# Performance work log

Measured on AMD Instinct MI355X. Metric: run time of the kernel, lower is better.

Reference implementation:

```python
import jax, jax.numpy as jnp
import numpy as np

B, S, H, NH, NKV, D = 1, 2048, 4096, 32, 8, 128
ROPE_BASE = 1000000.0


def setup_inputs() -> dict:
    key = jax.random.key(0)
    k0, k1, k2, k3, k4 = jax.random.split(key, 5)
    hidden_states = jax.random.normal(k0, (B, S, H), dtype=jnp.float32)
    Wq = jax.random.normal(k1, (NH * D, H), dtype=jnp.float32) * 0.02
    Wk = jax.random.normal(k2, (NKV * D, H), dtype=jnp.float32) * 0.02
    Wv = jax.random.normal(k3, (NKV * D, H), dtype=jnp.float32) * 0.02
    Wo = jax.random.normal(k4, (NH * D, NH * D), dtype=jnp.float32) * 0.02
    # RoPE tables (Mistral rope_theta = 1e6), concatenated-halves layout
    inv_freq = 1.0 / (ROPE_BASE ** (jnp.arange(0, D, 2, dtype=jnp.float32) / D))
    pos = jnp.arange(S, dtype=jnp.float32)
    freqs = pos[:, None] * inv_freq[None, :]            # [S, D/2]
    emb = jnp.concatenate([freqs, freqs], axis=-1)       # [S, D]
    cos = jnp.cos(emb)[None]                             # [1, S, D]
    sin = jnp.sin(emb)[None]
    # additive causal mask [1,1,S,S]
    causal = jnp.tril(jnp.ones((S, S), dtype=bool))
    attention_mask = jnp.where(causal, 0.0, -1e9).astype(jnp.float32)[None, None]
    return {"hidden_states": hidden_states, "cos": cos, "sin": sin,
            "attention_mask": attention_mask, "Wq": Wq, "Wk": Wk, "Wv": Wv, "Wo": Wo}


def _rotate_half(x):
    d = x.shape[-1] // 2
    return jnp.concatenate([-x[..., d:], x[..., :d]], axis=-1)


def reference(hidden_states, cos, sin, attention_mask, Wq, Wk, Wv, Wo):
    b, s, _ = hidden_states.shape
    nh = Wq.shape[0] // D
    nkv = Wk.shape[0] // D
    g = nh // nkv  # GQA groups
    scaling = D ** -0.5

    q = (hidden_states @ Wq.T).reshape(b, s, nh, D).transpose(0, 2, 1, 3)   # [b,nh,s,d]
    k = (hidden_states @ Wk.T).reshape(b, s, nkv, D).transpose(0, 2, 1, 3)  # [b,nkv,s,d]
    v = (hidden_states @ Wv.T).reshape(b, s, nkv, D).transpose(0, 2, 1, 3)

    c = cos[:, None]  # [b,1,s,d] broadcast over heads (unsqueeze_dim=1)
    sn = sin[:, None]
    q = q * c + _rotate_half(q) * sn
    k = k * c + _rotate_half(k) * sn

    # grouped-query attention without materializing repeated K/V
    qg = q.reshape(b, nkv, g, s, D)
    attn = jnp.einsum('bkgqd,bksd->bkgqs', qg, k) * scaling
    attn = attn + attention_mask[:, :, None]  # broadcast [1,1,1,s,s]
    w = jax.nn.softmax(attn.astype(jnp.float32), axis=-1).astype(q.dtype)
    out = jnp.einsum('bkgqs,bksd->bkgqd', w, v)  # [b,nkv,g,s,d]
    out = out.reshape(b, nh, s, D).transpose(0, 2, 1, 3).reshape(b, s, nh * D)
    return out @ Wo.T
```

## Files before the change

kernel.cpp:

```cpp
#include <hip/hip_runtime.h>
#include <hip/hip_bf16.h>
#include <cstdint>
#include <cstddef>

#define S_LEN 2048
#define HID   4096
#define NHEAD 32
#define NKVH  8
#define HD    128
#define QKV_STR 6144

typedef __bf16 bf16x8 __attribute__((ext_vector_type(8)));
typedef float  f32x4  __attribute__((ext_vector_type(4)));
typedef float  f32x16 __attribute__((ext_vector_type(16)));
typedef unsigned uint32x2_t __attribute__((ext_vector_type(2)));

__device__ __forceinline__ unsigned short f2bf(float f) {
  union { float f; unsigned int u; } c; c.f = f;
  unsigned int u = c.u;
  return (unsigned short)((u + 0x7fffu + ((u >> 16) & 1u)) >> 16);
}
__device__ __forceinline__ float bf2f(unsigned short b) {
  union { unsigned int u; float f; } c; c.u = ((unsigned int)b) << 16;
  return c.f;
}
__device__ __forceinline__ void gload16(const void* g, void* l) {
  __builtin_amdgcn_global_load_lds((const __attribute__((address_space(1))) void*)g,
                                   (__attribute__((address_space(3))) void*)l, 16, 0, 0);
}

__global__ void cvt_multi(const float* __restrict__ s0, const float* __restrict__ s1,
                          const float* __restrict__ s2, const float* __restrict__ s3,
                          unsigned short* __restrict__ d0, unsigned short* __restrict__ d1,
                          unsigned short* __restrict__ d2, unsigned short* __restrict__ d3,
                          int n0, int n1, int n2, int n3) {
  const float* src; unsigned short* dst; int n;
  switch (blockIdx.y) {
    case 0: src = s0; dst = d0; n = n0; break;
    case 1: src = s1; dst = d1; n = n1; break;
    case 2: src = s2; dst = d2; n = n2; break;
    default: src = s3; dst = d3; n = n3; break;
  }
  int i = blockIdx.x * blockDim.x + threadIdx.x;
  int stride = gridDim.x * blockDim.x;
  for (; i < n; i += stride) {
    float4 v = ((const float4*)src)[i];
    ushort4 o;
    o.x = f2bf(v.x); o.y = f2bf(v.y); o.z = f2bf(v.z); o.w = f2bf(v.w);
    ((ushort4*)dst)[i] = o;
  }
}

template <bool F32OUT>
__global__ __launch_bounds__(256)
void gemm_bt(const unsigned short* __restrict__ A,
             const unsigned short* __restrict__ Bm,
             void* __restrict__ Cout, int N, int K) {
  __shared__ __align__(16) unsigned short lA[3][128 * 32];
  __shared__ __align__(16) unsigned short lB[3][128 * 32];
  const int tid = threadIdx.x;
  const int lane = tid & 63, wid = tid >> 6;
  const int l15 = lane & 15, lg = lane >> 4;
  const int wr = (wid >> 1) * 64, wc = (wid & 1) * 64;
  const int nwg = gridDim.x * 16;
  int bid = blockIdx.x + blockIdx.y * gridDim.x;
  bid = (bid & 7) * (nwg >> 3) + (bid >> 3);
  const int bm = bid & 15, bn = bid >> 4;

  f32x4 acc[4][4] = {};
  const unsigned short* Ab = A + (size_t)bm * 128 * K;
  const unsigned short* Bb = Bm + (size_t)bn * 128 * K;

  auto stage = [&](int t, int buf) {
    const int k0 = t * 32;
#pragma unroll
    for (int i = 0; i < 2; ++i) {
      int c = tid + i * 256;
      int row = c >> 2, sl = c & 3;
      int g = sl ^ ((row >> 1) & 3);
      gload16(Ab + (size_t)row * K + k0 + g * 8, (char*)lA[buf] + c * 16);
      gload16(Bb + (size_t)row * K + k0 + g * 8, (char*)lB[buf] + c * 16);
    }
  };

  const int nt = K / 32;
  stage(0, 0);
  if (nt > 1) stage(1, 1);
  const int swz = (l15 >> 1) & 3;

  int cur = 0;
  for (int t = 0; t < nt; ++t) {
    if (t + 1 < nt) asm volatile("s_waitcnt vmcnt(4)" ::: "memory");
    else            asm volatile("s_waitcnt vmcnt(0)" ::: "memory");
    __builtin_amdgcn_s_barrier();
    __builtin_amdgcn_sched_barrier(0);
    if (t + 2 < nt) { int nb = cur + 2; if (nb >= 3) nb -= 3; stage(t + 2, nb); }
    bf16x8 af[4], bfr[4];
#pragma unroll
    for (int m = 0; m < 4; ++m)
      af[m] = *(const bf16x8*)&lA[cur][(wr + m * 16 + l15) * 32 + ((lg ^ swz) * 8)];
#pragma unroll
    for (int n = 0; n < 4; ++n)
      bfr[n] = *(const bf16x8*)&lB[cur][(wc + n * 16 + l15) * 32 + ((lg ^ swz) * 8)];
#pragma unroll
    for (int m = 0; m < 4; ++m)
#pragma unroll
      for (int n = 0; n < 4; ++n)
        acc[m][n] = __builtin_amdgcn_mfma_f32_16x16x32_bf16(af[m], bfr[n], acc[m][n], 0, 0, 0);
    ++cur; if (cur >= 3) cur -= 3;
  }
  const int r0 = bm * 128 + wr + 4 * lg;
  const int c0 = bn * 128 + wc + l15;
#pragma unroll
  for (int m = 0; m < 4; ++m)
#pragma unroll
    for (int n = 0; n < 4; ++n)
#pragma unroll
      for (int j = 0; j < 4; ++j) {
        size_t idx = (size_t)(r0 + m * 16 + j) * N + (c0 + n * 16);
        if (F32OUT) ((float*)Cout)[idx] = acc[m][n][j];
        else        ((unsigned short*)Cout)[idx] = f2bf(acc[m][n][j]);
      }
}

__global__ __launch_bounds__(256)
void rope_transpose(unsigned short* __restrict__ qkv,
                    const float* __restrict__ cp,
                    const float* __restrict__ sp,
                    unsigned short* __restrict__ VT) {
  __shared__ __align__(16) unsigned short tile[128 * 128];
  const int tid = threadIdx.x;
  const int s0 = blockIdx.x * 128;
  const int kvh = blockIdx.y;
  unsigned short* K = qkv + 4096 + kvh * 128;
#pragma unroll 4
  for (int i = 0; i < 32; ++i) {
    int idx = tid + i * 256;
    int sl = idx >> 6, d = idx & 63;
    float c = cp[(size_t)(s0 + sl) * 128 + d];
    float sn = sp[(size_t)(s0 + sl) * 128 + d];
    size_t base = (size_t)(s0 + sl) * QKV_STR + d;
    float x1 = bf2f(K[base]), x2 = bf2f(K[base + 64]);
    K[base]      = f2bf(x1 * c - x2 * sn);
    K[base + 64] = f2bf(x2 * c + x1 * sn);
  }
  const unsigned short* src = qkv + 5120 + kvh * 128;
#pragma unroll
  for (int i = 0; i < 8; ++i) {
    int c = tid + i * 256;
    int s = c >> 4, dc = c & 15;
    int f = (s ^ (s >> 3)) & 7;
    uint4 v = *(const uint4*)(src + (size_t)(s0 + s) * QKV_STR + dc * 8);
    *(uint4*)&tile[s * 128 + ((dc ^ f) * 8)] = v;
  }
  __syncthreads();
#pragma unroll
  for (int i = 0; i < 8; ++i) {
    int c = tid + i * 256;
    int d = c >> 4, sc = c & 15;
    unsigned short tmp[8];
#pragma unroll
    for (int j = 0; j < 8; ++j) {
      int s = sc * 8 + j;
      int f = (s ^ (s >> 3)) & 7;
      tmp[j] = tile[s * 128 + (((d >> 3) ^ f) * 8) + (d & 7)];
    }
    *(uint4*)(VT + ((size_t)kvh * 128 + d) * S_LEN + s0 + sc * 8) = *(uint4*)tmp;
  }
}

#define CROW(r) (((r) & 3) + 8 * ((r) >> 2) + 4 * hi)
__global__ __launch_bounds__(256, 2)
void flash_attn(const unsigned short* __restrict__ qkv,
                const unsigned short* __restrict__ VT,
                const float* __restrict__ cp,
                const float* __restrict__ sp,
                unsigned short* __restrict__ Og,
                const float* __restrict__ Wo,
                unsigned short* __restrict__ woB) {
  __shared__ __align__(16) unsigned short lK[2 * 64 * 128];
  __shared__ __align__(16) unsigned short lVt[2 * 128 * 64];
  const int tid = threadIdx.x;
  const int lane = tid & 63, w = tid >> 6;
  const int l31 = lane & 31, hi = lane >> 5;
  const int h = blockIdx.y, kvh = h >> 2;
  const int qt = (h & 16) ? blockIdx.x : (15 - blockIdx.x);
  const int nt = 2 * qt + 2;
  const int qminw = qt * 128 + w * 32;
  const int qlane = qminw + l31;
  const int qmaxw = qminw + 31;
  const float S2 = 0.12752960f;

  bf16x8 qf[8];
  {
    const unsigned short* qp = qkv + (size_t)qlane * QKV_STR + h * HD + hi * 8;
#pragma unroll
    for (int ks = 0; ks < 8; ++ks) qf[ks] = *(const bf16x8*)(qp + ks * 16);
    const float* crow = cp + (size_t)qlane * 128 + hi * 8;
    const float* srow = sp + (size_t)qlane * 128 + hi * 8;
#pragma unroll
    for (int ks = 0; ks < 4; ++ks) {
      float4 c0 = *(const float4*)(crow + ks * 16);
      float4 c1 = *(const float4*)(crow + ks * 16 + 4);
      float4 s0 = *(const float4*)(srow + ks * 16);
      float4 s1 = *(const float4*)(srow + ks * 16 + 4);
      float cc[8] = {c0.x, c0.y, c0.z, c0.w, c1.x, c1.y, c1.z, c1.w};
      float ss[8] = {s0.x, s0.y, s0.z, s0.w, s1.x, s1.y, s1.z, s1.w};
#pragma unroll
      for (int j = 0; j < 8; ++j) {
        float x1 = (float)qf[ks][j], x2 = (float)qf[ks + 4][j];
        qf[ks][j]     = (__bf16)(x1 * cc[j] - x2 * ss[j]);
        qf[ks + 4][j] = (__bf16)(x2 * cc[j] + x1 * ss[j]);
      }
    }
  }
  f32x16 accO[4] = {};
  float m_run = -3e38f, l_run = 0.f;

  const unsigned short* Kb0 = qkv + 4096 + kvh * HD;
  const unsigned short* VTh = VT + (size_t)kvh * 128 * S_LEN;

  auto stageK = [&](int t, int buf) {
    const unsigned short* Kb = Kb0 + (size_t)(t * 64) * QKV_STR;
    char* dst = (char*)(lK + buf * (64 * 128));
#pragma unroll
    for (int i = 0; i < 4; ++i) {
      int c = tid + i * 256;
      int row = c >> 4, s = c & 15;
      gload16(Kb + (size_t)row * QKV_STR + ((s ^ (row & 7)) * 8), dst + c * 16);
    }
  };
  auto stageV = [&](int t, int buf) {
    const unsigned short* Vb = VTh + t * 64;
    char* dst = (char*)(lVt + buf * (128 * 64));
#pragma unroll
    for (int i = 0; i < 4; ++i) {
      int c = tid + i * 256;
      int d = c >> 3, s = c & 7;
      gload16(Vb + (size_t)d * S_LEN + ((s ^ (d & 7)) * 8), dst + c * 16);
    }
  };

  stageK(0, 0);
  stageV(0, 0);
  __syncthreads();

  int cur = 0;
  for (int t = 0; t < nt; ++t) {
    const bool pf = (t + 1 < nt);
    if (pf) { stageK(t + 1, cur ^ 1); stageV(t + 1, cur ^ 1); }

#pragma unroll
    for (int c2 = 0; c2 < 2; ++c2) {
      const int kvb = t * 64 + c2 * 32;
      if (kvb > qmaxw) continue;
      f32x16 st = {};
      const unsigned short* lKc = lK + cur * (64 * 128) + c2 * 32 * 128;
      __builtin_amdgcn_s_setprio(1);
#pragma unroll
      for (int ks = 0; ks < 8; ++ks) {
        bf16x8 kf = *(const bf16x8*)&lKc[l31 * 128 + (((ks * 2 + hi) ^ (l31 & 7)) * 8)];
        st = __builtin_amdgcn_mfma_f32_32x32x16_bf16(kf, qf[ks], st, 0, 0, 0);
      }
      __builtin_amdgcn_s_setprio(0);
      if (kvb + 31 > qminw) {
#pragma unroll
        for (int r = 0; r < 16; ++r)
          if (kvb + CROW(r) > qlane) st[r] = -3e38f;
      }
      float t0 = fmaxf(st[0], st[1]),  t1 = fmaxf(st[2], st[3]);
      float t2 = fmaxf(st[4], st[5]),  t3 = fmaxf(st[6], st[7]);
      float t4 = fmaxf(st[8], st[9]),  t5 = fmaxf(st[10], st[11]);
      float t6 = fmaxf(st[12], st[13]), t7 = fmaxf(st[14], st[15]);
      float tm = fmaxf(fmaxf(fmaxf(t0, t1), fmaxf(t2, t3)),
                       fmaxf(fmaxf(t4, t5), fmaxf(t6, t7)));
      tm = fmaxf(tm, __shfl_xor(tm, 32));
      const bool skip = __all((tm - m_run) * S2 <= 8.0f);
      float corr = 1.f;
      if (!skip) {
        float mnew = fmaxf(m_run, tm);
        corr = __builtin_amdgcn_exp2f((m_run - mnew) * S2);
        m_run = mnew;
      }
      const float mS2 = m_run * S2;
      float p[16];
#pragma unroll
      for (int r = 0; r < 16; ++r) p[r] = __builtin_amdgcn_exp2f(st[r] * S2 - mS2);
      float s0b = (p[0] + p[1]) + (p[2] + p[3]);
      float s1b = (p[4] + p[5]) + (p[6] + p[7]);
      float s2b = (p[8] + p[9]) + (p[10] + p[11]);
      float s3b = (p[12] + p[13]) + (p[14] + p[15]);
      float rsum = (s0b + s1b) + (s2b + s3b);
      rsum += __shfl_xor(rsum, 32);
      l_run = l_run * corr + rsum;
      if (!skip) {
#pragma unroll
        for (int db = 0; db < 4; ++db) accO[db] = accO[db] * corr;
      }
      unsigned wpk[8];
#pragma unroll
      for (int i = 0; i < 8; ++i) {
        __hip_bfloat162 b2 = __float22bfloat162_rn(float2{p[2 * i], p[2 * i + 1]});
        wpk[i] = *(unsigned*)&b2;
      }
      int4 pa0i, pa1i;
#if __has_builtin(__builtin_amdgcn_permlane32_swap)
      uint32x2_t r0 = __builtin_amdgcn_permlane32_swap(wpk[0], wpk[2], false, false);
      uint32x2_t r1 = __builtin_amdgcn_permlane32_swap(wpk[1], wpk[3], false, false);
      uint32x2_t r2 = __builtin_amdgcn_permlane32_swap(wpk[4], wpk[6], false, false);
      uint32x2_t r3 = __builtin_amdgcn_permlane32_swap(wpk[5], wpk[7], false, false);
      pa0i.x = (int)r0.x; pa0i.y = (int)r1.x; pa0i.z = (int)r0.y; pa0i.w = (int)r1.y;
      pa1i.x = (int)r2.x; pa1i.y = (int)r3.x; pa1i.z = (int)r2.y; pa1i.w = (int)r3.y;
#else
      unsigned xpk[8];
#pragma unroll
      for (int i = 0; i < 8; ++i) xpk[i] = (unsigned)__shfl_xor((int)wpk[i], 32);
      pa0i.x = hi ? (int)xpk[2] : (int)wpk[0]; pa0i.y = hi ? (int)xpk[3] : (int)wpk[1];
      pa0i.z = hi ? (int)wpk[2] : (int)xpk[0]; pa0i.w = hi ? (int)wpk[3] : (int)xpk[1];
      pa1i.x = hi ? (int)xpk[6] : (int)wpk[4]; pa1i.y = hi ? (int)xpk[7] : (int)wpk[5];
      pa1i.z = hi ? (int)wpk[6] : (int)xpk[4]; pa1i.w = hi ? (int)wpk[7] : (int)xpk[5];
#endif
      bf16x8 pa0 = *(bf16x8*)&pa0i, pa1 = *(bf16x8*)&pa1i;
      const unsigned short* lVc = lVt + cur * (128 * 64);
      __builtin_amdgcn_s_setprio(1);
#pragma unroll
      for (int db = 0; db < 4; ++db) {
        int d = db * 32 + l31;
#pragma unroll
        for (int ks2 = 0; ks2 < 2; ++ks2) {
          int ck = c2 * 4 + ks2 * 2 + hi;
          bf16x8 vf = *(const bf16x8*)&lVc[d * 64 + ((ck ^ (d & 7)) * 8)];
          accO[db] = __builtin_amdgcn_mfma_f32_32x32x16_bf16(vf, ks2 ? pa1 : pa0, accO[db], 0, 0, 0);
        }
      }
      __builtin_amdgcn_s_setprio(0);
    }
    __syncthreads();
    cur ^= 1;
  }

  const float invl = 1.0f / l_run;
  unsigned short* orow = Og + (size_t)(qt * 128 + w * 32 + l31) * HID + h * HD;
#pragma unroll
  for (int db = 0; db < 4; ++db)
#pragma unroll
    for (int rr = 0; rr < 4; ++rr) {
      int d0 = db * 32 + rr * 8 + 4 * hi;
      ushort4 o;
      o.x = f2bf(accO[db][rr * 4 + 0] * invl);
      o.y = f2bf(accO[db][rr * 4 + 1] * invl);
      o.z = f2bf(accO[db][rr * 4 + 2] * invl);
      o.w = f2bf(accO[db][rr * 4 + 3] * invl);
      *(ushort4*)(orow + d0) = o;
    }

  {
    const int gb = blockIdx.y * gridDim.x + blockIdx.x;
    const int total = HID * HID / 4;
    for (int i = gb * 256 + tid; i < total; i += 512 * 256) {
      float4 v = ((const float4*)Wo)[i];
      ushort4 o;
      o.x = f2bf(v.x); o.y = f2bf(v.y); o.z = f2bf(v.z); o.w = f2bf(v.w);
      ((ushort4*)woB)[i] = o;
    }
  }
}

extern "C" void kernel_launch(void* const* d_in, const int* in_sizes, int n_in,
                              void* d_out, int out_size, void* d_ws, size_t ws_size,
                              hipStream_t stream) {
  const float* hs   = (const float*)d_in[0];
  const float* cosp = (const float*)d_in[1];
  const float* sinp = (const float*)d_in[2];
  const float* Wq = (const float*)d_in[4];
  const float* Wk = (const float*)d_in[5];
  const float* Wv = (const float*)d_in[6];
  const float* Wo = (const float*)d_in[7];
  float* out = (float*)d_out;

  uint8_t* ws = (uint8_t*)d_ws;
  size_t off = 0;
  auto alloc = [&](size_t bytes) { void* p = ws + off; off += bytes; return p; };
  unsigned short* hidB  = (unsigned short*)alloc((size_t)S_LEN * HID * 2);
  unsigned short* wqkvB = (unsigned short*)alloc((size_t)QKV_STR * HID * 2);
  unsigned short* woB   = (unsigned short*)alloc((size_t)HID * HID * 2);
  unsigned short* qkvB  = (unsigned short*)alloc((size_t)S_LEN * QKV_STR * 2);
  unsigned short* aoB   = (unsigned short*)alloc((size_t)S_LEN * HID * 2);
  unsigned short* vtB   = (unsigned short*)alloc((size_t)NKVH * HD * S_LEN * 2);

  cvt_multi<<<dim3(1024, 4), 256, 0, stream>>>(
      hs, Wq, Wk, Wv,
      hidB, wqkvB, wqkvB + (size_t)HID * HID, wqkvB + (size_t)(HID + 1024) * HID,
      S_LEN * HID / 4, HID * HID / 4, 1024 * HID / 4, 1024 * HID / 4);

  gemm_bt<false><<<dim3(QKV_STR / 128, S_LEN / 128), 256, 0, stream>>>(
      hidB, wqkvB, qkvB, QKV_STR, HID);

  rope_transpose<<<dim3(S_LEN / 128, NKVH), 256, 0, stream>>>(qkvB, cosp, sinp, vtB);

  flash_attn<<<dim3(S_LEN / 128, NHEAD), 256, 0, stream>>>(
      qkvB, vtB, cosp, sinp, aoB, Wo, woB);

  gemm_bt<true><<<dim3(HID / 128, S_LEN / 128), 256, 0, stream>>>(
      aoB, woB, out, HID, HID);
}
```

Baseline: 335.7 us.

## Fuse K RoPE and V transpose into QKV GEMM epilogue

Removes the separate rope_transpose kernel. In the QKV GEMM epilogue, tiles covering K columns stage the accumulators through shared memory and apply RoPE before storing, and tiles covering V columns write straight into the transposed VT layout. This saves one launch and a full read/write pass over K and V. In exchange the epilogue for those blocks gains extra shared-memory traffic and scattered cos/sin loads, and the V stores are 8-byte strided writes.

```diff
diff --git a/kernel.cpp b/kernel.cpp
--- a/kernel.cpp
+++ b/kernel.cpp
@@ -51,13 +51,16 @@
   }
 }
 
-template <bool F32OUT>
+template <bool F32OUT, bool EPIFUSE>
 __global__ __launch_bounds__(256)
 void gemm_bt(const unsigned short* __restrict__ A,
              const unsigned short* __restrict__ Bm,
-             void* __restrict__ Cout, int N, int K) {
-  __shared__ __align__(16) unsigned short lA[3][128 * 32];
-  __shared__ __align__(16) unsigned short lB[3][128 * 32];
+             void* __restrict__ Cout, int N, int K,
+             const float* __restrict__ cp, const float* __restrict__ sp,
+             unsigned short* __restrict__ VT) {
+  __shared__ __align__(16) unsigned short lsmem[2 * 3 * 128 * 32];
+  unsigned short (*lA)[128 * 32] = (unsigned short (*)[128 * 32])lsmem;
+  unsigned short (*lB)[128 * 32] = (unsigned short (*)[128 * 32])(lsmem + 3 * 128 * 32);
   const int tid = threadIdx.x;
   const int lane = tid & 63, wid = tid >> 6;
   const int l15 = lane & 15, lg = lane >> 4;
@@ -111,6 +114,55 @@
   }
   const int r0 = bm * 128 + wr + 4 * lg;
   const int c0 = bn * 128 + wc + l15;
+
+  if (EPIFUSE && bn >= 40) {
+    const int kvh = bn - 40;
+#pragma unroll
+    for (int n = 0; n < 4; ++n) {
+      int d = wc + n * 16 + l15;
+      unsigned short* vrow = VT + ((size_t)kvh * 128 + d) * S_LEN + bm * 128 + wr + 4 * lg;
+#pragma unroll
+      for (int m = 0; m < 4; ++m) {
+        ushort4 o;
+        o.x = f2bf(acc[m][n][0]); o.y = f2bf(acc[m][n][1]);
+        o.z = f2bf(acc[m][n][2]); o.w = f2bf(acc[m][n][3]);
+        *(ushort4*)(vrow + m * 16) = o;
+      }
+    }
+    return;
+  }
+  if (EPIFUSE && bn >= 32) {
+    __syncthreads();
+    unsigned short* scr = lsmem;
+    const int sl0 = wr + 4 * lg;
+#pragma unroll
+    for (int m = 0; m < 4; ++m)
+#pragma unroll
+      for (int n = 0; n < 4; ++n) {
+        int d = wc + n * 16 + l15;
+#pragma unroll
+        for (int j = 0; j < 4; ++j)
+          scr[(sl0 + m * 16 + j) * 128 + d] = f2bf(acc[m][n][j]);
+      }
+    __syncthreads();
+#pragma unroll
+    for (int m = 0; m < 4; ++m)
+#pragma unroll
+      for (int n = 0; n < 4; ++n) {
+        int d = wc + n * 16 + l15;
+#pragma unroll
+        for (int j = 0; j < 4; ++j) {
+          int sl = sl0 + m * 16 + j;
+          float x = bf2f(scr[sl * 128 + d]);
+          float pr = bf2f(scr[sl * 128 + (d ^ 64)]);
+          size_t crow = (size_t)(bm * 128 + sl) * 128 + (d & 63);
+          float c = cp[crow], sn = sp[crow];
+          float o = (d < 64) ? (x * c - pr * sn) : (x * c + pr * sn);
+          ((unsigned short*)Cout)[(size_t)(bm * 128 + sl) * N + bn * 128 + d] = f2bf(o);
+        }
+      }
+    return;
+  }
 #pragma unroll
   for (int m = 0; m < 4; ++m)
 #pragma unroll
@@ -121,52 +173,6 @@
         if (F32OUT) ((float*)Cout)[idx] = acc[m][n][j];
         else        ((unsigned short*)Cout)[idx] = f2bf(acc[m][n][j]);
       }
-}
-
-__global__ __launch_bounds__(256)
-void rope_transpose(unsigned short* __restrict__ qkv,
-                    const float* __restrict__ cp,
-                    const float* __restrict__ sp,
-                    unsigned short* __restrict__ VT) {
-  __shared__ __align__(16) unsigned short tile[128 * 128];
-  const int tid = threadIdx.x;
-  const int s0 = blockIdx.x * 128;
-  const int kvh = blockIdx.y;
-  unsigned short* K = qkv + 4096 + kvh * 128;
-#pragma unroll 4
-  for (int i = 0; i < 32; ++i) {
-    int idx = tid + i * 256;
-    int sl = idx >> 6, d = idx & 63;
-    float c = cp[(size_t)(s0 + sl) * 128 + d];
-    float sn = sp[(size_t)(s0 + sl) * 128 + d];
-    size_t base = (size_t)(s0 + sl) * QKV_STR + d;
-    float x1 = bf2f(K[base]), x2 = bf2f(K[base + 64]);
-    K[base]      = f2bf(x1 * c - x2 * sn);
-    K[base + 64] = f2bf(x2 * c + x1 * sn);
-  }
-  const unsigned short* src = qkv + 5120 + kvh * 128;
-#pragma unroll
-  for (int i = 0; i < 8; ++i) {
-    int c = tid + i * 256;
-    int s = c >> 4, dc = c & 15;
-    int f = (s ^ (s >> 3)) & 7;
-    uint4 v = *(const uint4*)(src + (size_t)(s0 + s) * QKV_STR + dc * 8);
-    *(uint4*)&tile[s * 128 + ((dc ^ f) * 8)] = v;
-  }
-  __syncthreads();
-#pragma unroll
-  for (int i = 0; i < 8; ++i) {
-    int c = tid + i * 256;
-    int d = c >> 4, sc = c & 15;
-    unsigned short tmp[8];
-#pragma unroll
-    for (int j = 0; j < 8; ++j) {
-      int s = sc * 8 + j;
-      int f = (s ^ (s >> 3)) & 7;
-      tmp[j] = tile[s * 128 + (((d >> 3) ^ f) * 8) + (d & 7)];
-    }
-    *(uint4*)(VT + ((size_t)kvh * 128 + d) * S_LEN + s0 + sc * 8) = *(uint4*)tmp;
-  }
 }
 
 #define CROW(r) (((r) & 3) + 8 * ((r) >> 2) + 4 * hi)
@@ -393,14 +399,12 @@
       hidB, wqkvB, wqkvB + (size_t)HID * HID, wqkvB + (size_t)(HID + 1024) * HID,
       S_LEN * HID / 4, HID * HID / 4, 1024 * HID / 4, 1024 * HID / 4);
 
-  gemm_bt<false><<<dim3(QKV_STR / 128, S_LEN / 128), 256, 0, stream>>>(
-      hidB, wqkvB, qkvB, QKV_STR, HID);
-
-  rope_transpose<<<dim3(S_LEN / 128, NKVH), 256, 0, stream>>>(qkvB, cosp, sinp, vtB);
+  gemm_bt<false, true><<<dim3(QKV_STR / 128, S_LEN / 128), 256, 0, stream>>>(
+      hidB, wqkvB, qkvB, QKV_STR, HID, cosp, sinp, vtB);
 
   flash_attn<<<dim3(S_LEN / 128, NHEAD), 256, 0, stream>>>(
       qkvB, vtB, cosp, sinp, aoB, Wo, woB);
 
-  gemm_bt<true><<<dim3(HID / 128, S_LEN / 128), 256, 0, stream>>>(
-      aoB, woB, out, HID, HID);
-}
+  gemm_bt<true, false><<<dim3(HID / 128, S_LEN / 128), 256, 0, stream>>>(
+      aoB, woB, out, HID, HID, nullptr, nullptr, nullptr);
+}
```

Measured after the change: 334.0 us. About the same (-0.5%).
